# Performance work log

Measured on AMD Instinct MI355X. Metric: run time of the kernel, lower is better.

## Reference

```python
import jax, jax.numpy as jnp
import numpy as np

EMD_DIM = 64
NB_EMD = 512


def setup_inputs() -> dict:
    key = jax.random.key(0)
    k_x, k_e = jax.random.split(key)
    x = jax.random.normal(k_x, (32, 64, 64, EMD_DIM), dtype=jnp.float32)
    # codebook buffer, shape [emd_dim, nb_emd] as in the torch module
    embed = jax.random.normal(k_e, (EMD_DIM, NB_EMD), dtype=jnp.float32)
    return {"x": x, "embed": embed}


def reference(x, embed):
    # Eval-mode forward (the EMA buffer update only runs under self.training
    # and does not affect this forward's outputs).
    flatten = x.reshape(-1, EMD_DIM)                      # [N, d]
    dist = (jnp.sum(flatten * flatten, axis=1, keepdims=True)
            - 2.0 * flatten @ embed
            + jnp.sum(embed * embed, axis=0, keepdims=True))  # [N, K]
    emd_id_flat = jnp.argmax(-dist, axis=1)               # nearest code index [N]
    emd_id = emd_id_flat.reshape(x.shape[:-1])            # [B, H, W]
    q = jnp.take(embed.T, emd_id, axis=0)                 # gather codes -> [B,H,W,d]
    diff = jnp.mean((jax.lax.stop_gradient(q) - x) ** 2)  # commitment loss
    q_st = x + jax.lax.stop_gradient(q - x)               # straight-through
    return (q_st, diff, emd_id)
```

## Files before the change

kernel.cpp:

```cpp
#include <hip/hip_runtime.h>

#define N_VEC 131072
#define K 512
#define D 64
#define GUARD 0.05f
#define NB_GATHER 2048
#define FB_Q 16

typedef __attribute__((ext_vector_type(8))) short bf16x8;
typedef __attribute__((ext_vector_type(4))) float f32x4;

static __device__ __forceinline__ short f2bf(float f) {
  unsigned u = __builtin_bit_cast(unsigned, f);
  u += 0x7fffu + ((u >> 16) & 1u);
  return (short)(u >> 16);
}
static __device__ __forceinline__ float bf2f(short h) {
  unsigned u = ((unsigned)(unsigned short)h) << 16;
  return __builtin_bit_cast(float, u);
}
static __device__ __forceinline__ void split8(const float4 f0, const float4 f1,
                                              bf16x8& h, bf16x8& m) {
  const float v[8] = {f0.x, f0.y, f0.z, f0.w, f1.x, f1.y, f1.z, f1.w};
#pragma unroll
  for (int j = 0; j < 8; ++j) {
    const short hh = f2bf(v[j]);
    h[j] = hh;
    m[j] = f2bf(v[j] - bf2f(hh));
  }
}

__global__ __launch_bounds__(64) void vq_prep_kernel(
    const float* __restrict__ embed, float* __restrict__ et,
    float* __restrict__ nrm, bf16x8* __restrict__ F, int* __restrict__ cnt)
{
  const int b = blockIdx.x;
  const int lane = threadIdx.x;
  if (b < 32) {
    const int row = lane & 15;
    const int kg  = lane >> 4;
    const int code = b * 16 + row;
#pragma unroll
    for (int c = 0; c < 2; ++c) {
      bf16x8 h, m;
#pragma unroll
      for (int j = 0; j < 8; ++j) {
        const int d = kg * 8 + c * 32 + j;
        const float e = embed[d * K + code];
        const short hh = f2bf(e);
        h[j] = hh;
        m[j] = f2bf(e - bf2f(hh));
      }
      F[b * 256 + c * 128 + 0  + lane] = h;
      F[b * 256 + c * 128 + 64 + lane] = m;
    }
  } else {
    if (b == 32 && lane == 0) cnt[0] = 0;
    const int code = (b - 32) * 64 + lane;
    float s = 0.f;
#pragma unroll
    for (int d = 0; d < D; ++d) {
      const float e = embed[d * K + code];
      et[code * D + d] = e;
      s = fmaf(e, e, s);
    }
    nrm[code] = s;
  }
}

#define MFMA12(P0, Q0, P1, Q1, BH0, BM0, BH1, BM1) do {                        \
    P0 = __builtin_amdgcn_mfma_f32_16x16x32_bf16(Ah0c0, BH0, kZero, 0, 0, 0); \
    P1 = __builtin_amdgcn_mfma_f32_16x16x32_bf16(Ah1c0, BH0, kZero, 0, 0, 0); \
    Q0 = __builtin_amdgcn_mfma_f32_16x16x32_bf16(Ah0c1, BM1, kZero, 0, 0, 0); \
    Q1 = __builtin_amdgcn_mfma_f32_16x16x32_bf16(Ah1c1, BM1, kZero, 0, 0, 0); \
    P0 = __builtin_amdgcn_mfma_f32_16x16x32_bf16(Ah0c1, BH1, P0, 0, 0, 0);    \
    P1 = __builtin_amdgcn_mfma_f32_16x16x32_bf16(Ah1c1, BH1, P1, 0, 0, 0);    \
    Q0 = __builtin_amdgcn_mfma_f32_16x16x32_bf16(Am0c0, BH0, Q0, 0, 0, 0);    \
    Q1 = __builtin_amdgcn_mfma_f32_16x16x32_bf16(Am1c0, BH0, Q1, 0, 0, 0);    \
    P0 = __builtin_amdgcn_mfma_f32_16x16x32_bf16(Ah0c0, BM0, P0, 0, 0, 0);    \
    P1 = __builtin_amdgcn_mfma_f32_16x16x32_bf16(Ah1c0, BM0, P1, 0, 0, 0);    \
    Q0 = __builtin_amdgcn_mfma_f32_16x16x32_bf16(Am0c1, BH1, Q0, 0, 0, 0);    \
    Q1 = __builtin_amdgcn_mfma_f32_16x16x32_bf16(Am1c1, BH1, Q1, 0, 0, 0);    \
  } while (0)

#define SCORE4(P0, Q0, P1, Q1, CODE, NV) do {                                  \
    _Pragma("unroll")                                                          \
    for (int r = 0; r < 4; ++r) {                                              \
      const float s0 = fmaf(-2.f, P0[r], fmaf(-2.f, Q0[r], (NV)));             \
      b2[r] = __builtin_amdgcn_fmed3f(s0, b1[r], b2[r]);                       \
      if (s0 < b1[r]) { b1[r] = s0; i1[r] = (CODE); }                          \
      const float s1 = fmaf(-2.f, P1[r], fmaf(-2.f, Q1[r], (NV)));             \
      b2[4 + r] = __builtin_amdgcn_fmed3f(s1, b1[4 + r], b2[4 + r]);           \
      if (s1 < b1[4 + r]) { b1[4 + r] = s1; i1[4 + r] = (CODE); }              \
    }                                                                          \
  } while (0)

__global__ __launch_bounds__(512, 4) void vq_coarse_kernel(
    const float* __restrict__ x, const bf16x8* __restrict__ F,
    const float* __restrict__ nrm, float* __restrict__ idf,
    int* __restrict__ cnt, int* __restrict__ list)
{
  __shared__ bf16x8 LB[4096];
  const int tid  = threadIdx.x;
  const int lane = tid & 63;
  const int w    = tid >> 6;
  const int row  = lane & 15;
  const int kg   = lane >> 4;
  const int qbase = blockIdx.x * 256 + w * 32;

  bf16x8 Ah0c0, Ah0c1, Ah1c0, Ah1c1, Am0c0, Am0c1, Am1c0, Am1c1;
  {
    const float* xr0 = x + (size_t)(qbase + row) * D + kg * 8;
    const float* xr1 = x + (size_t)(qbase + 16 + row) * D + kg * 8;
    split8(*reinterpret_cast<const float4*>(xr0),
           *reinterpret_cast<const float4*>(xr0 + 4), Ah0c0, Am0c0);
    split8(*reinterpret_cast<const float4*>(xr0 + 32),
           *reinterpret_cast<const float4*>(xr0 + 36), Ah0c1, Am0c1);
    split8(*reinterpret_cast<const float4*>(xr1),
           *reinterpret_cast<const float4*>(xr1 + 4), Ah1c0, Am1c0);
    split8(*reinterpret_cast<const float4*>(xr1 + 32),
           *reinterpret_cast<const float4*>(xr1 + 36), Ah1c1, Am1c1);
  }

  float b1[8], b2[8]; int i1[8];
#pragma unroll
  for (int r = 0; r < 8; ++r) { b1[r] = 3.4e38f; b2[r] = 3.4e38f; i1[r] = 0; }

  const f32x4 kZero = {0.f, 0.f, 0.f, 0.f};

#pragma unroll 1
  for (int ph = 0; ph < 2; ++ph) {
    if (ph) __syncthreads();
    {
      const float4* src = reinterpret_cast<const float4*>(F + ph * 4096);
      float4* dst = reinterpret_cast<float4*>(LB);
#pragma unroll
      for (int j = 0; j < 8; ++j) dst[tid + j * 512] = src[tid + j * 512];
    }
    __syncthreads();

#pragma unroll 4
    for (int t = 0; t < 16; ++t) {
      const bf16x8 Bh0 = LB[t * 256 + lane];
      const bf16x8 Bm0 = LB[t * 256 + 64 + lane];
      const bf16x8 Bh1 = LB[t * 256 + 128 + lane];
      const bf16x8 Bm1 = LB[t * 256 + 192 + lane];
      const int code = (ph * 16 + t) * 16 + row;
      const float nv = nrm[code];
      f32x4 p0, q0, p1, q1;
      MFMA12(p0, q0, p1, q1, Bh0, Bm0, Bh1, Bm1);
      SCORE4(p0, q0, p1, q1, code, nv);
    }
  }

#pragma unroll
  for (int m = 1; m < 16; m <<= 1) {
#pragma unroll
    for (int r = 0; r < 8; ++r) {
      const float o1 = __shfl_xor(b1[r], m, 64);
      const int   oi = __shfl_xor(i1[r], m, 64);
      const float o2 = __shfl_xor(b2[r], m, 64);
      if (o1 < b1[r]) { b2[r] = fminf(b1[r], o2); b1[r] = o1; i1[r] = oi; }
      else            { b2[r] = fminf(b2[r], o1); }
    }
  }

  unsigned m32 = 0;
  if (row == 0) {
#pragma unroll
    for (int r = 0; r < 8; ++r) {
      const int qoff = (r >> 2) * 16 + kg * 4 + (r & 3);
      idf[qbase + qoff] = (float)i1[r];
      if (b2[r] - b1[r] < GUARD) m32 |= 1u << qoff;
    }
  }
  m32 |= __shfl_xor((int)m32, 16, 64);
  m32 |= __shfl_xor((int)m32, 32, 64);
  if (lane == 0 && m32) {
    int base = atomicAdd(cnt, __popc(m32));
    while (m32) {
      const int b = __ffs(m32) - 1;
      m32 &= m32 - 1;
      list[base++] = qbase + b;
    }
  }
}

__global__ __launch_bounds__(256) void vq_fallback_kernel(
    const float* __restrict__ x, const float* __restrict__ embed,
    const float* __restrict__ nrm, const int* __restrict__ cnt,
    const int* __restrict__ list, float* __restrict__ idf)
{
  __shared__ float x_lds[FB_Q * D];
  __shared__ int   s_qidx[FB_Q];
  __shared__ float s_best[4][FB_Q];
  __shared__ int   s_bid[4][FB_Q];
  const int tid  = threadIdx.x;
  const int lane = tid & 63;
  const int wv   = tid >> 6;
  const int n = cnt[0];

  for (int qb = blockIdx.x * FB_Q; qb < n; qb += gridDim.x * FB_Q) {
    __syncthreads();
    if (tid < FB_Q) {
      const int idx = qb + tid;
      s_qidx[tid] = list[idx < n ? idx : qb];
    }
    __syncthreads();
    {
      const int qj = tid >> 4, dq = tid & 15;
      *reinterpret_cast<float4*>(&x_lds[qj * D + dq * 4]) =
          *reinterpret_cast<const float4*>(x + (size_t)s_qidx[qj] * D + dq * 4);
    }
    __syncthreads();

    const int c0 = wv * 128 + lane;
    const int c1 = c0 + 64;
    float a0[FB_Q], a1[FB_Q];
#pragma unroll
    for (int i = 0; i < FB_Q; ++i) { a0[i] = 0.f; a1[i] = 0.f; }

#pragma unroll 4
    for (int ch = 0; ch < 16; ++ch) {
      const int d0 = ch * 4;
      const float e00 = embed[(d0 + 0) * K + c0];
      const float e01 = embed[(d0 + 0) * K + c1];
      const float e10 = embed[(d0 + 1) * K + c0];
      const float e11 = embed[(d0 + 1) * K + c1];
      const float e20 = embed[(d0 + 2) * K + c0];
      const float e21 = embed[(d0 + 2) * K + c1];
      const float e30 = embed[(d0 + 3) * K + c0];
      const float e31 = embed[(d0 + 3) * K + c1];
#pragma unroll
      for (int i = 0; i < FB_Q; ++i) {
        const float4 xv = *reinterpret_cast<const float4*>(&x_lds[i * D + d0]);
        a0[i] = fmaf(xv.x, e00, a0[i]);
        a0[i] = fmaf(xv.y, e10, a0[i]);
        a0[i] = fmaf(xv.z, e20, a0[i]);
        a0[i] = fmaf(xv.w, e30, a0[i]);
        a1[i] = fmaf(xv.x, e01, a1[i]);
        a1[i] = fmaf(xv.y, e11, a1[i]);
        a1[i] = fmaf(xv.z, e21, a1[i]);
        a1[i] = fmaf(xv.w, e31, a1[i]);
      }
    }

    const float nr0 = nrm[c0], nr1 = nrm[c1];
#pragma unroll
    for (int i = 0; i < FB_Q; ++i) {
      float best; int bid;
      const float s0 = fmaf(-2.f, a0[i], nr0);
      best = s0; bid = c0;
      const float s1 = fmaf(-2.f, a1[i], nr1);
      if (s1 < best) { best = s1; bid = c1; }
#pragma unroll
      for (int off = 32; off > 0; off >>= 1) {
        const float s2 = __shfl_down(best, off, 64);
        const int   b2 = __shfl_down(bid, off, 64);
        if (s2 < best || (s2 == best && b2 < bid)) { best = s2; bid = b2; }
      }
      if (lane == 0) { s_best[wv][i] = best; s_bid[wv][i] = bid; }
    }
    __syncthreads();
    if (tid < FB_Q) {
      float best = s_best[0][tid]; int bid = s_bid[0][tid];
#pragma unroll
      for (int w = 1; w < 4; ++w) {
        const float s = s_best[w][tid];
        if (s < best) { best = s; bid = s_bid[w][tid]; }
      }
      idf[s_qidx[tid]] = (float)bid;
    }
  }
}

__global__ __launch_bounds__(256) void vq_gather_kernel(
    const float* __restrict__ x, const float* __restrict__ et,
    const float* __restrict__ idf, float* __restrict__ q,
    float* __restrict__ partial)
{
  const int tid = blockIdx.x * 256 + threadIdx.x;
  const int stride = gridDim.x * 256;
  float acc = 0.f;
  for (int idx = tid; idx < N_VEC * (D / 4); idx += stride) {
    const int v = idx >> 4;
    const int d4 = idx & 15;
    const int id = (int)idf[v];
    const float4 xv = reinterpret_cast<const float4*>(x)[idx];
    const float4 ev = reinterpret_cast<const float4*>(et)[(id << 4) + d4];
    const float e0 = ev.x - xv.x, e1 = ev.y - xv.y, e2 = ev.z - xv.z, e3 = ev.w - xv.w;
    acc += (e0 * e0 + e1 * e1) + (e2 * e2 + e3 * e3);
    reinterpret_cast<float4*>(q)[idx] = ev;
  }
  acc += __shfl_down(acc, 32, 64);
  acc += __shfl_down(acc, 16, 64);
  acc += __shfl_down(acc, 8, 64);
  acc += __shfl_down(acc, 4, 64);
  acc += __shfl_down(acc, 2, 64);
  acc += __shfl_down(acc, 1, 64);
  __shared__ float sred[4];
  if ((threadIdx.x & 63) == 0) sred[threadIdx.x >> 6] = acc;
  __syncthreads();
  if (threadIdx.x == 0)
    partial[blockIdx.x] = (sred[0] + sred[1]) + (sred[2] + sred[3]);
}

__global__ __launch_bounds__(256) void vq_finalize_kernel(
    const float* __restrict__ partial, float* __restrict__ out)
{
  float acc = 0.f;
  for (int i = threadIdx.x; i < NB_GATHER; i += 256) acc += partial[i];
  acc += __shfl_down(acc, 32, 64);
  acc += __shfl_down(acc, 16, 64);
  acc += __shfl_down(acc, 8, 64);
  acc += __shfl_down(acc, 4, 64);
  acc += __shfl_down(acc, 2, 64);
  acc += __shfl_down(acc, 1, 64);
  __shared__ float sred[4];
  if ((threadIdx.x & 63) == 0) sred[threadIdx.x >> 6] = acc;
  __syncthreads();
  if (threadIdx.x == 0)
    out[0] = ((sred[0] + sred[1]) + (sred[2] + sred[3])) * (1.0f / (float)(N_VEC * D));
}

extern "C" void kernel_launch(void* const* d_in, const int* in_sizes, int n_in,
                              void* d_out, int out_size, void* d_ws, size_t ws_size,
                              hipStream_t stream) {
  const float* x = (const float*)d_in[0];
  const float* embed = (const float*)d_in[1];
  float* out = (float*)d_out;
  float* q    = out;
  float* diff = out + 8388608;
  float* idf  = out + 8388609;

  float* ws = (float*)d_ws;
  float* et      = ws;
  float* nrm     = ws + 32768;
  float* partial = ws + 33312;
  int*   cnt     = (int*)(ws + 35360);
  int*   list    = (int*)(ws + 35368);
  bf16x8* F = (bf16x8*)(ws + 35368 + N_VEC);

  vq_prep_kernel<<<40, 64, 0, stream>>>(embed, et, nrm, F, cnt);
  vq_coarse_kernel<<<N_VEC / 256, 512, 0, stream>>>(x, F, nrm, idf, cnt, list);
  vq_fallback_kernel<<<1024, 256, 0, stream>>>(x, embed, nrm, cnt, list, idf);
  vq_gather_kernel<<<NB_GATHER, 256, 0, stream>>>(x, et, idf, q, partial);
  vq_finalize_kernel<<<1, 256, 0, stream>>>(partial, diff);
}
```

Baseline: 80.77 us.

## Shrink coarse VQ tile to 16 queries per wave with smaller LDS stages

Each wave in the coarse distance kernel now handles 16 query rows instead of 32, and the codebook is staged through LDS in four 32 KB phases instead of two 64 KB ones. The grid doubles and the launch bound asks for 8 waves per SIMD, with waves starting at staggered LDS tile offsets. The aim is higher occupancy, fewer registers and fewer LDS bank conflicts. The cost is that each loaded codebook tile is reused by half as many queries, so LDS and global traffic per query roughly double, and there are more barriers.

```diff
diff --git a/kernel.cpp b/kernel.cpp
--- a/kernel.cpp
+++ b/kernel.cpp
@@ -68,95 +68,75 @@
   }
 }
 
-#define MFMA12(P0, Q0, P1, Q1, BH0, BM0, BH1, BM1) do {                        \
-    P0 = __builtin_amdgcn_mfma_f32_16x16x32_bf16(Ah0c0, BH0, kZero, 0, 0, 0); \
-    P1 = __builtin_amdgcn_mfma_f32_16x16x32_bf16(Ah1c0, BH0, kZero, 0, 0, 0); \
-    Q0 = __builtin_amdgcn_mfma_f32_16x16x32_bf16(Ah0c1, BM1, kZero, 0, 0, 0); \
-    Q1 = __builtin_amdgcn_mfma_f32_16x16x32_bf16(Ah1c1, BM1, kZero, 0, 0, 0); \
-    P0 = __builtin_amdgcn_mfma_f32_16x16x32_bf16(Ah0c1, BH1, P0, 0, 0, 0);    \
-    P1 = __builtin_amdgcn_mfma_f32_16x16x32_bf16(Ah1c1, BH1, P1, 0, 0, 0);    \
-    Q0 = __builtin_amdgcn_mfma_f32_16x16x32_bf16(Am0c0, BH0, Q0, 0, 0, 0);    \
-    Q1 = __builtin_amdgcn_mfma_f32_16x16x32_bf16(Am1c0, BH0, Q1, 0, 0, 0);    \
-    P0 = __builtin_amdgcn_mfma_f32_16x16x32_bf16(Ah0c0, BM0, P0, 0, 0, 0);    \
-    P1 = __builtin_amdgcn_mfma_f32_16x16x32_bf16(Ah1c0, BM0, P1, 0, 0, 0);    \
-    Q0 = __builtin_amdgcn_mfma_f32_16x16x32_bf16(Am0c1, BH1, Q0, 0, 0, 0);    \
-    Q1 = __builtin_amdgcn_mfma_f32_16x16x32_bf16(Am1c1, BH1, Q1, 0, 0, 0);    \
-  } while (0)
-
-#define SCORE4(P0, Q0, P1, Q1, CODE, NV) do {                                  \
-    _Pragma("unroll")                                                          \
-    for (int r = 0; r < 4; ++r) {                                              \
-      const float s0 = fmaf(-2.f, P0[r], fmaf(-2.f, Q0[r], (NV)));             \
-      b2[r] = __builtin_amdgcn_fmed3f(s0, b1[r], b2[r]);                       \
-      if (s0 < b1[r]) { b1[r] = s0; i1[r] = (CODE); }                          \
-      const float s1 = fmaf(-2.f, P1[r], fmaf(-2.f, Q1[r], (NV)));             \
-      b2[4 + r] = __builtin_amdgcn_fmed3f(s1, b1[4 + r], b2[4 + r]);           \
-      if (s1 < b1[4 + r]) { b1[4 + r] = s1; i1[4 + r] = (CODE); }              \
-    }                                                                          \
-  } while (0)
-
-__global__ __launch_bounds__(512, 4) void vq_coarse_kernel(
+__global__ __launch_bounds__(512, 8) void vq_coarse_kernel(
     const float* __restrict__ x, const bf16x8* __restrict__ F,
     const float* __restrict__ nrm, float* __restrict__ idf,
     int* __restrict__ cnt, int* __restrict__ list)
 {
-  __shared__ bf16x8 LB[4096];
+  __shared__ bf16x8 LB[2048];
   const int tid  = threadIdx.x;
   const int lane = tid & 63;
   const int w    = tid >> 6;
   const int row  = lane & 15;
   const int kg   = lane >> 4;
-  const int qbase = blockIdx.x * 256 + w * 32;
-
-  bf16x8 Ah0c0, Ah0c1, Ah1c0, Ah1c1, Am0c0, Am0c1, Am1c0, Am1c1;
+  const int qbase = blockIdx.x * 128 + w * 16;
+
+  bf16x8 Ah0c0, Ah0c1, Am0c0, Am0c1;
   {
     const float* xr0 = x + (size_t)(qbase + row) * D + kg * 8;
-    const float* xr1 = x + (size_t)(qbase + 16 + row) * D + kg * 8;
     split8(*reinterpret_cast<const float4*>(xr0),
            *reinterpret_cast<const float4*>(xr0 + 4), Ah0c0, Am0c0);
     split8(*reinterpret_cast<const float4*>(xr0 + 32),
            *reinterpret_cast<const float4*>(xr0 + 36), Ah0c1, Am0c1);
-    split8(*reinterpret_cast<const float4*>(xr1),
-           *reinterpret_cast<const float4*>(xr1 + 4), Ah1c0, Am1c0);
-    split8(*reinterpret_cast<const float4*>(xr1 + 32),
-           *reinterpret_cast<const float4*>(xr1 + 36), Ah1c1, Am1c1);
-  }
-
-  float b1[8], b2[8]; int i1[8];
-#pragma unroll
-  for (int r = 0; r < 8; ++r) { b1[r] = 3.4e38f; b2[r] = 3.4e38f; i1[r] = 0; }
+  }
+
+  float b1[4], b2[4]; int i1[4];
+#pragma unroll
+  for (int r = 0; r < 4; ++r) { b1[r] = 3.4e38f; b2[r] = 3.4e38f; i1[r] = 0; }
 
   const f32x4 kZero = {0.f, 0.f, 0.f, 0.f};
 
 #pragma unroll 1
-  for (int ph = 0; ph < 2; ++ph) {
+  for (int ph = 0; ph < 4; ++ph) {
     if (ph) __syncthreads();
     {
-      const float4* src = reinterpret_cast<const float4*>(F + ph * 4096);
+      const float4* src = reinterpret_cast<const float4*>(F + ph * 2048);
       float4* dst = reinterpret_cast<float4*>(LB);
 #pragma unroll
-      for (int j = 0; j < 8; ++j) dst[tid + j * 512] = src[tid + j * 512];
-    }
-    __syncthreads();
-
-#pragma unroll 4
-    for (int t = 0; t < 16; ++t) {
-      const bf16x8 Bh0 = LB[t * 256 + lane];
-      const bf16x8 Bm0 = LB[t * 256 + 64 + lane];
-      const bf16x8 Bh1 = LB[t * 256 + 128 + lane];
-      const bf16x8 Bm1 = LB[t * 256 + 192 + lane];
-      const int code = (ph * 16 + t) * 16 + row;
+      for (int j = 0; j < 4; ++j) dst[tid + j * 512] = src[tid + j * 512];
+    }
+    __syncthreads();
+
+#pragma unroll
+    for (int t = 0; t < 8; ++t) {
+      const int tt = (t + w) & 7;
+      const int base = tt * 256;
+      const bf16x8 Bh0 = LB[base + lane];
+      const bf16x8 Bm0 = LB[base + 64 + lane];
+      const bf16x8 Bh1 = LB[base + 128 + lane];
+      const bf16x8 Bm1 = LB[base + 192 + lane];
+      const int code = (ph * 8 + tt) * 16 + row;
       const float nv = nrm[code];
-      f32x4 p0, q0, p1, q1;
-      MFMA12(p0, q0, p1, q1, Bh0, Bm0, Bh1, Bm1);
-      SCORE4(p0, q0, p1, q1, code, nv);
+      f32x4 P, Q;
+      P = __builtin_amdgcn_mfma_f32_16x16x32_bf16(Ah0c0, Bh0, kZero, 0, 0, 0);
+      Q = __builtin_amdgcn_mfma_f32_16x16x32_bf16(Ah0c1, Bm1, kZero, 0, 0, 0);
+      P = __builtin_amdgcn_mfma_f32_16x16x32_bf16(Ah0c1, Bh1, P, 0, 0, 0);
+      Q = __builtin_amdgcn_mfma_f32_16x16x32_bf16(Am0c0, Bh0, Q, 0, 0, 0);
+      P = __builtin_amdgcn_mfma_f32_16x16x32_bf16(Ah0c0, Bm0, P, 0, 0, 0);
+      Q = __builtin_amdgcn_mfma_f32_16x16x32_bf16(Am0c1, Bh1, Q, 0, 0, 0);
+#pragma unroll
+      for (int r = 0; r < 4; ++r) {
+        const float s0 = fmaf(-2.f, P[r], fmaf(-2.f, Q[r], nv));
+        b2[r] = __builtin_amdgcn_fmed3f(s0, b1[r], b2[r]);
+        if (s0 < b1[r]) { b1[r] = s0; i1[r] = code; }
+      }
     }
   }
 
 #pragma unroll
   for (int m = 1; m < 16; m <<= 1) {
 #pragma unroll
-    for (int r = 0; r < 8; ++r) {
+    for (int r = 0; r < 4; ++r) {
       const float o1 = __shfl_xor(b1[r], m, 64);
       const int   oi = __shfl_xor(i1[r], m, 64);
       const float o2 = __shfl_xor(b2[r], m, 64);
@@ -165,22 +145,22 @@
     }
   }
 
-  unsigned m32 = 0;
+  unsigned m16 = 0;
   if (row == 0) {
 #pragma unroll
-    for (int r = 0; r < 8; ++r) {
-      const int qoff = (r >> 2) * 16 + kg * 4 + (r & 3);
+    for (int r = 0; r < 4; ++r) {
+      const int qoff = kg * 4 + r;
       idf[qbase + qoff] = (float)i1[r];
-      if (b2[r] - b1[r] < GUARD) m32 |= 1u << qoff;
-    }
-  }
-  m32 |= __shfl_xor((int)m32, 16, 64);
-  m32 |= __shfl_xor((int)m32, 32, 64);
-  if (lane == 0 && m32) {
-    int base = atomicAdd(cnt, __popc(m32));
-    while (m32) {
-      const int b = __ffs(m32) - 1;
-      m32 &= m32 - 1;
+      if (b2[r] - b1[r] < GUARD) m16 |= 1u << qoff;
+    }
+  }
+  m16 |= __shfl_xor((int)m16, 16, 64);
+  m16 |= __shfl_xor((int)m16, 32, 64);
+  if (lane == 0 && m16) {
+    int base = atomicAdd(cnt, __popc(m16));
+    while (m16) {
+      const int b = __ffs(m16) - 1;
+      m16 &= m16 - 1;
       list[base++] = qbase + b;
     }
   }
@@ -342,7 +322,7 @@
   bf16x8* F = (bf16x8*)(ws + 35368 + N_VEC);
 
   vq_prep_kernel<<<40, 64, 0, stream>>>(embed, et, nrm, F, cnt);
-  vq_coarse_kernel<<<N_VEC / 256, 512, 0, stream>>>(x, F, nrm, idf, cnt, list);
+  vq_coarse_kernel<<<N_VEC / 128, 512, 0, stream>>>(x, F, nrm, idf, cnt, list);
   vq_fallback_kernel<<<1024, 256, 0, stream>>>(x, embed, nrm, cnt, list, idf);
   vq_gather_kernel<<<NB_GATHER, 256, 0, stream>>>(x, et, idf, q, partial);
   vq_finalize_kernel<<<1, 256, 0, stream>>>(partial, diff);
```

After: 112.9 us. 1.4x slower.
